# Kernel tuning notes

Measured on AMD Instinct MI355X. Metric: run time of the kernel, lower is better.

The kernel has to match this reference:

```python
import jax, jax.numpy as jnp
import numpy as np

B, N, D = 4, 1024, 1024
H, DH = 16, 64            # heads, dim_head; inner_dim = H*DH = D
CTX_N, CTX_D = 77, 768    # CLIP text context
FF_IN, FF_HID = 8 * D, 4 * D  # GEGLU: proj to 2*4*D, gate to 4*D
EPS = 1e-5
SCALE = DH ** -0.5
NL = 256                  # 2**8 levels for all quantizers
ZP_QKV = 128.0            # asymmetric 8-bit zero point for q/k/v
ZP_W = 0.0                # always_zero=True for softmax-weight quantizer


def _round_ste(t):
    return t + jax.lax.stop_gradient(jnp.round(t) - t)


def _fake_quant(x, delta, zp):
    xq = jnp.clip(_round_ste(x / delta) + zp, 0.0, NL - 1.0)
    return (xq - zp) * delta


def _ln(x, w, b):
    m = x.mean(-1, keepdims=True)
    v = x.var(-1, keepdims=True)
    return (x - m) * jax.lax.rsqrt(v + EPS) * w + b


def _split_heads(t):  # [b, n, h*d] -> [b, h, n, d]
    b, n, _ = t.shape
    return t.reshape(b, n, H, DH).transpose(0, 2, 1, 3)


def _attn(x, ctx, wq, wk, wv, wo, bo, dq, dk, dv, dw):
    q = _split_heads(x @ wq)
    k = _split_heads(ctx @ wk)
    v = _split_heads(ctx @ wv)
    qq = _fake_quant(q, dq, ZP_QKV)
    kk = _fake_quant(k, dk, ZP_QKV)
    sim = jnp.einsum('bhid,bhjd->bhij', qq, kk) * SCALE
    attn = jax.nn.softmax(sim, axis=-1)
    aw = _fake_quant(attn, dw, ZP_W)
    vv = _fake_quant(v, dv, ZP_QKV)
    out = jnp.einsum('bhij,bhjd->bhid', aw, vv)
    b, _, n, _ = out.shape
    out = out.transpose(0, 2, 1, 3).reshape(b, n, H * DH)
    return out @ wo + bo


def _geglu_ff(x, w1, b1, w2, b2):
    h = x @ w1 + b1
    a, g = jnp.split(h, 2, axis=-1)
    return (a * jax.nn.gelu(g, approximate=False)) @ w2 + b2


def setup_inputs() -> dict:
    key = jax.random.key(0)
    ks = jax.random.split(key, 16)
    w = lambda i, shp, s: jax.random.normal(ks[i], shp, jnp.float32) * s
    sD = D ** -0.5
    sC = CTX_D ** -0.5
    return {
        'x': jax.random.normal(ks[0], (B, N, D), jnp.float32),
        'context': jax.random.normal(ks[1], (B, CTX_N, CTX_D), jnp.float32),
        'norm1_w': jnp.ones((D,), jnp.float32), 'norm1_b': jnp.zeros((D,), jnp.float32),
        'norm2_w': jnp.ones((D,), jnp.float32), 'norm2_b': jnp.zeros((D,), jnp.float32),
        'norm3_w': jnp.ones((D,), jnp.float32), 'norm3_b': jnp.zeros((D,), jnp.float32),
        'a1_wq': w(2, (D, D), sD), 'a1_wk': w(3, (D, D), sD), 'a1_wv': w(4, (D, D), sD),
        'a1_wo': w(5, (D, D), sD), 'a1_bo': jnp.zeros((D,), jnp.float32),
        'a2_wq': w(6, (D, D), sD), 'a2_wk': w(7, (CTX_D, D), sC), 'a2_wv': w(8, (CTX_D, D), sC),
        'a2_wo': w(9, (D, D), sD), 'a2_bo': jnp.zeros((D,), jnp.float32),
        'ff_w1': w(10, (D, FF_IN), sD), 'ff_b1': jnp.zeros((FF_IN,), jnp.float32),
        'ff_w2': w(11, (FF_HID, D), FF_HID ** -0.5), 'ff_b2': jnp.zeros((D,), jnp.float32),
        'd1_q': jnp.asarray(0.02, jnp.float32), 'd1_k': jnp.asarray(0.02, jnp.float32),
        'd1_v': jnp.asarray(0.02, jnp.float32), 'd1_w': jnp.asarray(1.0 / 255.0, jnp.float32),
        'd2_q': jnp.asarray(0.02, jnp.float32), 'd2_k': jnp.asarray(0.02, jnp.float32),
        'd2_v': jnp.asarray(0.02, jnp.float32), 'd2_w': jnp.asarray(1.0 / 255.0, jnp.float32),
    }


def reference(x, context, norm1_w, norm1_b, norm2_w, norm2_b, norm3_w, norm3_b,
              a1_wq, a1_wk, a1_wv, a1_wo, a1_bo,
              a2_wq, a2_wk, a2_wv, a2_wo, a2_bo,
              ff_w1, ff_b1, ff_w2, ff_b2,
              d1_q, d1_k, d1_v, d1_w, d2_q, d2_k, d2_v, d2_w):
    # attn1: quantized self-attention
    x = _attn(_ln(x, norm1_w, norm1_b), _ln(x, norm1_w, norm1_b),
              a1_wq, a1_wk, a1_wv, a1_wo, a1_bo, d1_q, d1_k, d1_v, d1_w) + x
    # attn2: quantized cross-attention with text context
    x = _attn(_ln(x, norm2_w, norm2_b), context,
              a2_wq, a2_wk, a2_wv, a2_wo, a2_bo, d2_q, d2_k, d2_v, d2_w) + x
    # GEGLU feed-forward
    x = _geglu_ff(_ln(x, norm3_w, norm3_b), ff_w1, ff_b1, ff_w2, ff_b2) + x
    return x
```

## Files before the change

kernel.cpp:

```cpp
#include <hip/hip_runtime.h>
#include <math.h>


typedef unsigned short u16;
typedef __attribute__((ext_vector_type(8))) short short8;
typedef __attribute__((ext_vector_type(4))) float f32x4;

__device__ inline float b2f(u16 v) { return __uint_as_float(((unsigned)v) << 16); }
__device__ inline u16 f2b(float f) {
  unsigned u = __float_as_uint(f);
  unsigned r = u + 0x7fffu + ((u >> 16) & 1u);
  return (u16)(r >> 16);
}

__device__ inline void glds16(const u16* g, u16* l) {
  __builtin_amdgcn_global_load_lds(
      (const __attribute__((address_space(1))) void*)g,
      (__attribute__((address_space(3))) void*)l, 16, 0, 0);
}

__global__ __launch_bounds__(256) void transpose_k(const float* __restrict__ in,
                                                   u16* __restrict__ out,
                                                   int R, int C) {
  __shared__ float t[32][33];
  int tx = threadIdx.x & 31, ty = threadIdx.x >> 5;
  int c0 = blockIdx.x * 32, r0 = blockIdx.y * 32;
#pragma unroll
  for (int i = 0; i < 32; i += 8)
    t[ty + i][tx] = in[(size_t)(r0 + ty + i) * C + c0 + tx];
  __syncthreads();
#pragma unroll
  for (int i = 0; i < 32; i += 8)
    out[(size_t)(c0 + ty + i) * R + r0 + tx] = f2b(t[tx][ty + i]);
}

struct TrBatch { const float* in[4]; u16* out[4]; int R[4]; };
__global__ __launch_bounds__(256) void transpose4_k(TrBatch a) {
  int z = blockIdx.z;
  const float* in = a.in[z];
  u16* out = a.out[z];
  int R = a.R[z];
  int r0 = blockIdx.y * 32;
  if (r0 >= R) return;
  __shared__ float t[32][33];
  int tx = threadIdx.x & 31, ty = threadIdx.x >> 5;
  int c0 = blockIdx.x * 32;
#pragma unroll
  for (int i = 0; i < 32; i += 8)
    t[ty + i][tx] = in[(size_t)(r0 + ty + i) * 1024 + c0 + tx];
  __syncthreads();
#pragma unroll
  for (int i = 0; i < 32; i += 8)
    out[(size_t)(c0 + ty + i) * R + r0 + tx] = f2b(t[tx][ty + i]);
}

__global__ __launch_bounds__(256) void tr16_k(const u16* __restrict__ in,
                                              u16* __restrict__ out, int NK,
                                              int NKP) {
  __shared__ u16 t[32][33];
  int tx = threadIdx.x & 31, ty = threadIdx.x >> 5;
  int n0 = blockIdx.x * 32, c0 = blockIdx.y * 32, b = blockIdx.z;
  const u16* ib = in + (size_t)b * NK * 1024;
  u16* ob = out + (size_t)b * 1024 * NKP;
#pragma unroll
  for (int i = 0; i < 32; i += 8) {
    int n = n0 + ty + i;
    n = n < NK ? n : NK - 1;
    t[ty + i][tx] = ib[(size_t)n * 1024 + c0 + tx];
  }
  __syncthreads();
#pragma unroll
  for (int i = 0; i < 32; i += 8)
    ob[(size_t)(c0 + ty + i) * NKP + n0 + tx] = t[tx][ty + i];
}

__global__ __launch_bounds__(256) void cast_k(const float* __restrict__ in,
                                              u16* __restrict__ out) {
  int i = (blockIdx.x * 256 + threadIdx.x) * 4;
  float4 v = *(const float4*)(in + i);
  out[i + 0] = f2b(v.x);
  out[i + 1] = f2b(v.y);
  out[i + 2] = f2b(v.z);
  out[i + 3] = f2b(v.w);
}

__global__ __launch_bounds__(256) void ln_k(const float* __restrict__ X,
                                            const float* __restrict__ W,
                                            const float* __restrict__ Bi,
                                            u16* __restrict__ Out) {
  const int row = blockIdx.x, tid = threadIdx.x;
  float4 x = *(const float4*)(X + (size_t)row * 1024 + tid * 4);
  float s = x.x + x.y + x.z + x.w;
  float s2 = x.x * x.x + x.y * x.y + x.z * x.z + x.w * x.w;
#pragma unroll
  for (int off = 32; off >= 1; off >>= 1) {
    s += __shfl_down(s, off);
    s2 += __shfl_down(s2, off);
  }
  __shared__ float red[8];
  int wave = tid >> 6, lane = tid & 63;
  if (lane == 0) { red[wave] = s; red[4 + wave] = s2; }
  __syncthreads();
  s = red[0] + red[1] + red[2] + red[3];
  s2 = red[4] + red[5] + red[6] + red[7];
  float mean = s * 0.0009765625f;
  float var = s2 * 0.0009765625f - mean * mean;
  float rs = rsqrtf(var + 1e-5f);
  float4 w = *(const float4*)(W + tid * 4);
  float4 b = *(const float4*)(Bi + tid * 4);
  u16* orow = Out + (size_t)row * 1024 + tid * 4;
  orow[0] = f2b((x.x - mean) * rs * w.x + b.x);
  orow[1] = f2b((x.y - mean) * rs * w.y + b.y);
  orow[2] = f2b((x.z - mean) * rs * w.z + b.z);
  orow[3] = f2b((x.w - mean) * rs * w.w + b.w);
}

template <int EPI, int TM>
__global__ __launch_bounds__(256, 2) void gemm_bt(
    const u16* __restrict__ A, int lda, const u16* __restrict__ Bt, int ldb,
    void* __restrict__ Cp, int ldc, const float* __restrict__ bias,
    const float* __restrict__ res, int ldr, const float* __restrict__ dp,
    const float* __restrict__ dp2, const float* __restrict__ dp3,
    size_t segsz, int M, int N, int K) {
  __shared__ __align__(16) u16 As[TM * 64];
  __shared__ __align__(16) u16 Bs[128 * 64];
  const int tid = threadIdx.x;
  const int lane = tid & 63, wave = tid >> 6;
  const int qd = lane >> 4, cl = lane & 15;
  const int wm = (wave & 1) * (TM / 2), wn = (wave >> 1) << 6;
  const int m0 = blockIdx.x * TM, n0 = blockIdx.y * 128;

  f32x4 acc[TM / 32][4];
  const f32x4 zero = {0.f, 0.f, 0.f, 0.f};
#pragma unroll
  for (int i = 0; i < TM / 32; i++)
#pragma unroll
    for (int j = 0; j < 4; j++) acc[i][j] = zero;

  for (int k0 = 0; k0 < K; k0 += 64) {
    __syncthreads();
#pragma unroll
    for (int it = 0; it < TM / 32; ++it) {
      int ch = it * 256 + tid;
      int r = ch >> 3, cc = (ch & 7) << 3;
      int gr = m0 + r;
      gr = gr < M ? gr : M - 1;
      glds16(A + (size_t)gr * lda + k0 + cc, As + ch * 8);
    }
#pragma unroll
    for (int it = 0; it < 4; ++it) {
      int ch = it * 256 + tid;
      int r = ch >> 3, cc = (ch & 7) << 3;
      glds16(Bt + (size_t)(n0 + r) * ldb + k0 + cc, Bs + ch * 8);
    }
    __syncthreads();
#pragma unroll
    for (int ks = 0; ks < 64; ks += 32) {
      short8 af[TM / 32], bf[4];
#pragma unroll
      for (int t = 0; t < TM / 32; t++)
        af[t] = *(const short8*)(As + (wm + t * 16 + cl) * 64 + ks + qd * 8);
#pragma unroll
      for (int t = 0; t < 4; t++)
        bf[t] = *(const short8*)(Bs + (wn + t * 16 + cl) * 64 + ks + qd * 8);
#pragma unroll
      for (int mt = 0; mt < TM / 32; mt++)
#pragma unroll
        for (int nt = 0; nt < 4; nt++)
          acc[mt][nt] = __builtin_amdgcn_mfma_f32_16x16x32_bf16(
              af[mt], bf[nt], acc[mt][nt], 0, 0, 0);
    }
  }

  float dscale = 1.f;
  u16* qbase = (u16*)Cp;
  if constexpr (EPI == 0) dscale = 1.0f / dp[0];
  if constexpr (EPI == 2) {
    int seg = n0 >> 10;
    const float* ds = (seg == 0) ? dp : ((seg == 1) ? dp2 : dp3);
    dscale = 1.0f / ds[0];
    qbase = (u16*)Cp + (size_t)seg * segsz;
  }
#pragma unroll
  for (int mt = 0; mt < TM / 32; ++mt) {
#pragma unroll
    for (int r = 0; r < 4; ++r) {
      int row = m0 + wm + mt * 16 + qd * 4 + r;
      if (row >= M) continue;
#pragma unroll
      for (int nt = 0; nt < 4; ++nt) {
        int col = n0 + wn + nt * 16 + cl;
        float v = acc[mt][nt][r];
        if constexpr (EPI == 0) {
          float xq = rintf(v * dscale) + 128.f;
          xq = fminf(fmaxf(xq, 0.f), 255.f);
          qbase[(size_t)row * ldc + col] = f2b(xq - 128.f);
        } else if constexpr (EPI == 2) {
          float xq = rintf(v * dscale) + 128.f;
          xq = fminf(fmaxf(xq, 0.f), 255.f);
          qbase[(size_t)row * ldc + (col & 1023)] = f2b(xq - 128.f);
        } else {
          v += bias[col] + res[(size_t)row * ldr + col];
          ((float*)Cp)[(size_t)row * ldc + col] = v;
        }
      }
    }
  }
}

__global__ __launch_bounds__(256, 2) void ff1_geglu_k(
    const u16* __restrict__ A, const u16* __restrict__ W1t,
    const float* __restrict__ b1, u16* __restrict__ gg, int M) {
  __shared__ __align__(16) u16 As[128 * 64];
  __shared__ __align__(16) u16 Ba[64 * 64];
  __shared__ __align__(16) u16 Bg[64 * 64];
  const int tid = threadIdx.x;
  const int lane = tid & 63, wave = tid >> 6;
  const int qd = lane >> 4, cl = lane & 15;
  const int wm = (wave & 1) << 6, wn = (wave >> 1) << 5;
  const int m0 = blockIdx.x * 128, n0 = blockIdx.y * 64;

  f32x4 aca[4][2], acg[4][2];
  const f32x4 zero = {0.f, 0.f, 0.f, 0.f};
#pragma unroll
  for (int i = 0; i < 4; i++)
#pragma unroll
    for (int j = 0; j < 2; j++) { aca[i][j] = zero; acg[i][j] = zero; }

  for (int k0 = 0; k0 < 1024; k0 += 64) {
    __syncthreads();
#pragma unroll
    for (int it = 0; it < 4; ++it) {
      int ch = it * 256 + tid;
      int r = ch >> 3, cc = (ch & 7) << 3;
      glds16(A + (size_t)(m0 + r) * 1024 + k0 + cc, As + ch * 8);
    }
#pragma unroll
    for (int it = 0; it < 2; ++it) {
      int ch = it * 256 + tid;
      int r = ch >> 3, cc = (ch & 7) << 3;
      glds16(W1t + (size_t)(n0 + r) * 1024 + k0 + cc, Ba + ch * 8);
      glds16(W1t + (size_t)(4096 + n0 + r) * 1024 + k0 + cc, Bg + ch * 8);
    }
    __syncthreads();
#pragma unroll
    for (int ks = 0; ks < 64; ks += 32) {
      short8 af[4], ba[2], bg[2];
#pragma unroll
      for (int t = 0; t < 4; t++)
        af[t] = *(const short8*)(As + (wm + t * 16 + cl) * 64 + ks + qd * 8);
#pragma unroll
      for (int t = 0; t < 2; t++) {
        ba[t] = *(const short8*)(Ba + (wn + t * 16 + cl) * 64 + ks + qd * 8);
        bg[t] = *(const short8*)(Bg + (wn + t * 16 + cl) * 64 + ks + qd * 8);
      }
#pragma unroll
      for (int mt = 0; mt < 4; mt++)
#pragma unroll
        for (int nt = 0; nt < 2; nt++) {
          aca[mt][nt] = __builtin_amdgcn_mfma_f32_16x16x32_bf16(
              af[mt], ba[nt], aca[mt][nt], 0, 0, 0);
          acg[mt][nt] = __builtin_amdgcn_mfma_f32_16x16x32_bf16(
              af[mt], bg[nt], acg[mt][nt], 0, 0, 0);
        }
    }
  }
#pragma unroll
  for (int mt = 0; mt < 4; ++mt)
#pragma unroll
    for (int r = 0; r < 4; ++r) {
      int row = m0 + wm + mt * 16 + qd * 4 + r;
#pragma unroll
      for (int nt = 0; nt < 2; ++nt) {
        int col = n0 + wn + nt * 16 + cl;
        float a = aca[mt][nt][r] + b1[col];
        float g = acg[mt][nt][r] + b1[4096 + col];
        float ge = 0.5f * g * (1.0f + erff(g * 0.70710678118654752f));
        gg[(size_t)row * 4096 + col] = f2b(a * ge);
      }
    }
}

__global__ __launch_bounds__(256, 4) void attn_k(
    const u16* __restrict__ Q, const u16* __restrict__ Kb,
    const u16* __restrict__ VbT, u16* __restrict__ O,
    const float* dqp, const float* dkp, const float* dvp, const float* dwp,
    int NK, int NKP) {
  __shared__ __align__(16) u16 Ks[64 * 64];
  __shared__ __align__(16) u16 VTs[64 * 64];
  __shared__ __align__(16) u16 Ps[4][16 * 72];
  const int tid = threadIdx.x;
  const int lane = tid & 63, wave = tid >> 6;
  const int qd = lane >> 4, cl = lane & 15;
  const int b = blockIdx.z, h = blockIdx.y, qt = blockIdx.x;
  const float sscale = dqp[0] * dkp[0] * 0.125f;
  const float oscale = dwp[0] * dvp[0];
  const float inv_dw = 1.0f / dwp[0];
  const f32x4 zero = {0.f, 0.f, 0.f, 0.f};

  short8 qf[2][2];
#pragma unroll
  for (int g = 0; g < 2; ++g) {
    const u16* qrow =
        Q + (size_t)(b * 1024 + qt * 128 + g * 64 + wave * 16 + cl) * 1024 +
        h * 64;
    qf[g][0] = *(const short8*)(qrow + qd * 8);
    qf[g][1] = *(const short8*)(qrow + 32 + qd * 8);
  }

  const u16* kbase = Kb + (size_t)(b * NK) * 1024 + h * 64;
  const u16* vtbase = VbT + ((size_t)b * 1024 + h * 64) * NKP;
  const int r_st = tid >> 3, c_st = (tid & 7) << 3;

  float m_s[2] = {-1e30f, -1e30f}, l_s[2] = {0.f, 0.f};
  for (int j0 = 0; j0 < NK; j0 += 64) {
    __syncthreads();
#pragma unroll
    for (int it = 0; it < 2; ++it) {
      int r = it * 32 + r_st;
      int j = j0 + r;
      j = j < NK ? j : NK - 1;
      glds16(kbase + (size_t)j * 1024 + c_st, Ks + (it * 256 + tid) * 8);
    }
    __syncthreads();
    const bool full = (j0 + 64 <= NK);
#pragma unroll
    for (int g = 0; g < 2; ++g) {
      float sc[16];
#pragma unroll
      for (int nt = 0; nt < 4; ++nt) {
        short8 kf0 = *(const short8*)(Ks + (nt * 16 + cl) * 64 + qd * 8);
        short8 kf1 = *(const short8*)(Ks + (nt * 16 + cl) * 64 + 32 + qd * 8);
        f32x4 st = zero;
        st = __builtin_amdgcn_mfma_f32_16x16x32_bf16(kf0, qf[g][0], st, 0, 0, 0);
        st = __builtin_amdgcn_mfma_f32_16x16x32_bf16(kf1, qf[g][1], st, 0, 0, 0);
#pragma unroll
        for (int r = 0; r < 4; ++r) {
          int key = j0 + nt * 16 + qd * 4 + r;
          sc[nt * 4 + r] = (full || key < NK) ? st[r] * sscale : -1e30f;
        }
      }
      float mx = sc[0];
#pragma unroll
      for (int i = 1; i < 16; ++i) mx = fmaxf(mx, sc[i]);
      mx = fmaxf(mx, __shfl_xor(mx, 16));
      mx = fmaxf(mx, __shfl_xor(mx, 32));
      float mn = fmaxf(m_s[g], mx);
      float ss = 0.f;
#pragma unroll
      for (int i = 0; i < 16; ++i) ss += __expf(sc[i] - mn);
      ss += __shfl_xor(ss, 16);
      ss += __shfl_xor(ss, 32);
      l_s[g] = l_s[g] * __expf(m_s[g] - mn) + ss;
      m_s[g] = mn;
    }
  }
  float il_s[2] = {1.0f / l_s[0], 1.0f / l_s[1]};

  f32x4 oacc[2][4];
#pragma unroll
  for (int g = 0; g < 2; ++g)
#pragma unroll
    for (int t = 0; t < 4; t++) oacc[g][t] = zero;

  for (int j0 = 0; j0 < NK; j0 += 64) {
    __syncthreads();
#pragma unroll
    for (int it = 0; it < 2; ++it) {
      int r = it * 32 + r_st;
      int j = j0 + r;
      j = j < NK ? j : NK - 1;
      glds16(kbase + (size_t)j * 1024 + c_st, Ks + (it * 256 + tid) * 8);
      glds16(vtbase + (size_t)r * NKP + j0 + c_st, VTs + (it * 256 + tid) * 8);
    }
    __syncthreads();
    const bool full = (j0 + 64 <= NK);
#pragma unroll
    for (int g = 0; g < 2; ++g) {
#pragma unroll
      for (int nt = 0; nt < 4; ++nt) {
        short8 kf0 = *(const short8*)(Ks + (nt * 16 + cl) * 64 + qd * 8);
        short8 kf1 = *(const short8*)(Ks + (nt * 16 + cl) * 64 + 32 + qd * 8);
        f32x4 st = zero;
        st = __builtin_amdgcn_mfma_f32_16x16x32_bf16(kf0, qf[g][0], st, 0, 0, 0);
        st = __builtin_amdgcn_mfma_f32_16x16x32_bf16(kf1, qf[g][1], st, 0, 0, 0);
        u16 pk[4];
#pragma unroll
        for (int r = 0; r < 4; ++r) {
          int key = j0 + nt * 16 + qd * 4 + r;
          float aw = 0.f;
          if (full || key < NK) {
            float attn = __expf(st[r] * sscale - m_s[g]) * il_s[g];
            aw = fminf(fmaxf(rintf(attn * inv_dw), 0.f), 255.f);
          }
          pk[r] = f2b(aw);
        }
        uint2 pv;
        pv.x = (unsigned)pk[0] | ((unsigned)pk[1] << 16);
        pv.y = (unsigned)pk[2] | ((unsigned)pk[3] << 16);
        *(uint2*)(&Ps[wave][cl * 72 + nt * 16 + qd * 4]) = pv;
      }
#pragma unroll
      for (int ks = 0; ks < 2; ++ks) {
        short8 pf = *(const short8*)(&Ps[wave][cl * 72 + ks * 32 + qd * 8]);
#pragma unroll
        for (int dt = 0; dt < 4; ++dt) {
          short8 vf =
              *(const short8*)(VTs + (dt * 16 + cl) * 64 + ks * 32 + qd * 8);
          oacc[g][dt] = __builtin_amdgcn_mfma_f32_16x16x32_bf16(
              pf, vf, oacc[g][dt], 0, 0, 0);
        }
      }
    }
  }
#pragma unroll
  for (int g = 0; g < 2; ++g)
#pragma unroll
    for (int dt = 0; dt < 4; ++dt)
#pragma unroll
      for (int r = 0; r < 4; r++) {
        size_t addr = (size_t)(b * 1024 + qt * 128 + g * 64 + wave * 16 +
                               qd * 4 + r) * 1024 +
                      h * 64 + dt * 16 + cl;
        O[addr] = f2b(oacc[g][dt][r] * oscale);
      }
}

extern "C" void kernel_launch(void* const* d_in, const int* in_sizes, int n_in,
                              void* d_out, int out_size, void* d_ws,
                              size_t ws_size, hipStream_t stream) {
  (void)in_sizes; (void)n_in; (void)out_size; (void)ws_size;
  const float* x    = (const float*)d_in[0];
  const float* ctx  = (const float*)d_in[1];
  const float* n1w  = (const float*)d_in[2];
  const float* n1b  = (const float*)d_in[3];
  const float* n2w  = (const float*)d_in[4];
  const float* n2b  = (const float*)d_in[5];
  const float* n3w  = (const float*)d_in[6];
  const float* n3b  = (const float*)d_in[7];
  const float* a1wq = (const float*)d_in[8];
  const float* a1wk = (const float*)d_in[9];
  const float* a1wv = (const float*)d_in[10];
  const float* a1wo = (const float*)d_in[11];
  const float* a1bo = (const float*)d_in[12];
  const float* a2wq = (const float*)d_in[13];
  const float* a2wk = (const float*)d_in[14];
  const float* a2wv = (const float*)d_in[15];
  const float* a2wo = (const float*)d_in[16];
  const float* a2bo = (const float*)d_in[17];
  const float* ffw1 = (const float*)d_in[18];
  const float* ffb1 = (const float*)d_in[19];
  const float* ffw2 = (const float*)d_in[20];
  const float* ffb2 = (const float*)d_in[21];
  const float* d1q = (const float*)d_in[22];
  const float* d1k = (const float*)d_in[23];
  const float* d1v = (const float*)d_in[24];
  const float* d1w = (const float*)d_in[25];
  const float* d2q = (const float*)d_in[26];
  const float* d2k = (const float*)d_in[27];
  const float* d2v = (const float*)d_in[28];
  const float* d2w = (const float*)d_in[29];

  char* ws = (char*)d_ws;
  const size_t MB = 1u << 20;
  u16* W    = (u16*)(ws + 0 * MB);
  u16* lnb  = (u16*)(ws + 16 * MB);
  u16* qb   = (u16*)(ws + 24 * MB);
  u16* kb   = (u16*)(ws + 32 * MB);
  u16* vb   = (u16*)(ws + 40 * MB);
  u16* vbT  = (u16*)(ws + 48 * MB);
  u16* ao   = (u16*)(ws + 56 * MB);
  float* x1 = (float*)(ws + 64 * MB);
  u16* k2b  = (u16*)(ws + 32 * MB);
  u16* v2b  = k2b + 308 * 1024;
  u16* vbTc = (u16*)(ws + 34 * MB);
  u16* ctxb = (u16*)(ws + 35 * MB);
  u16* gg   = (u16*)(ws + 24 * MB);

  u16* WT0 = W;
  u16* WT1 = (u16*)(ws + 2 * MB);
  u16* WT2 = (u16*)(ws + 4 * MB);
  u16* WT3 = (u16*)(ws + 6 * MB);
  u16* WT3c = WT2 + 1024 * 768;

  dim3 T256(256);
  {
    TrBatch tb;
    tb.in[0] = a1wq; tb.out[0] = WT0; tb.R[0] = 1024;
    tb.in[1] = a1wk; tb.out[1] = WT1; tb.R[1] = 1024;
    tb.in[2] = a1wv; tb.out[2] = WT2; tb.R[2] = 1024;
    tb.in[3] = a1wo; tb.out[3] = WT3; tb.R[3] = 1024;
    transpose4_k<<<dim3(32, 32, 4), T256, 0, stream>>>(tb);
  }
  ln_k<<<4096, T256, 0, stream>>>(x, n1w, n1b, lnb);
  gemm_bt<2, 128><<<dim3(32, 24), T256, 0, stream>>>(
      lnb, 1024, WT0, 1024, qb, 1024, nullptr, nullptr, 0, d1q, d1k, d1v,
      (size_t)4096 * 1024, 4096, 3072, 1024);
  tr16_k<<<dim3(32, 32, 4), T256, 0, stream>>>(vb, vbT, 1024, 1024);
  attn_k<<<dim3(8, 16, 4), T256, 0, stream>>>(qb, kb, vbT, ao, d1q, d1k, d1v,
                                              d1w, 1024, 1024);
  gemm_bt<1, 64><<<dim3(64, 8), T256, 0, stream>>>(
      ao, 1024, WT3, 1024, x1, 1024, a1bo, x, 1024, nullptr, nullptr, nullptr,
      0, 4096, 1024, 1024);
  {
    TrBatch tb;
    tb.in[0] = a2wq; tb.out[0] = WT0; tb.R[0] = 1024;
    tb.in[1] = a2wo; tb.out[1] = WT1; tb.R[1] = 1024;
    tb.in[2] = a2wk; tb.out[2] = WT2;  tb.R[2] = 768;
    tb.in[3] = a2wv; tb.out[3] = WT3c; tb.R[3] = 768;
    transpose4_k<<<dim3(32, 32, 4), T256, 0, stream>>>(tb);
  }
  ln_k<<<4096, T256, 0, stream>>>(x1, n2w, n2b, lnb);
  cast_k<<<231, T256, 0, stream>>>(ctx, ctxb);
  gemm_bt<0, 64><<<dim3(64, 8), T256, 0, stream>>>(
      lnb, 1024, WT0, 1024, qb, 1024, nullptr, nullptr, 0, d2q, nullptr,
      nullptr, 0, 4096, 1024, 1024);
  gemm_bt<2, 64><<<dim3(5, 16), T256, 0, stream>>>(
      ctxb, 768, WT2, 768, k2b, 1024, nullptr, nullptr, 0, d2k, d2v, nullptr,
      (size_t)308 * 1024, 308, 2048, 768);
  tr16_k<<<dim3(3, 32, 4), T256, 0, stream>>>(v2b, vbTc, 77, 128);
  attn_k<<<dim3(8, 16, 4), T256, 0, stream>>>(qb, k2b, vbTc, ao, d2q, d2k, d2v,
                                              d2w, 77, 128);
  gemm_bt<1, 64><<<dim3(64, 8), T256, 0, stream>>>(
      ao, 1024, WT1, 1024, x1, 1024, a2bo, x1, 1024, nullptr, nullptr, nullptr,
      0, 4096, 1024, 1024);
  transpose_k<<<dim3(256, 32), T256, 0, stream>>>(ffw1, W, 1024, 8192);
  ln_k<<<4096, T256, 0, stream>>>(x1, n3w, n3b, lnb);
  ff1_geglu_k<<<dim3(32, 64), T256, 0, stream>>>(lnb, W, ffb1, gg, 4096);
  transpose_k<<<dim3(32, 128), T256, 0, stream>>>(ffw2, W, 4096, 1024);
  gemm_bt<1, 64><<<dim3(64, 8), T256, 0, stream>>>(
      gg, 4096, W, 4096, d_out, 1024, ffb2, x1, 1024, nullptr, nullptr,
      nullptr, 0, 4096, 1024, 4096);
}
```

Before: 586.6 us.

## Rewrite GEGLU FF1 GEMM as 256x256 tile double-buffered 8-wave pipelined kernel

Replaces the 128x64 (plus gate) FF1 GEGLU kernel with a 512-thread kernel that computes a 256-row by 128-value/128-gate tile. It double-buffers A and B in 128 KB of LDS, interleaving global-to-LDS loads for the next K tile with MFMA quadrants. It uses XOR-swizzled LDS layouts to avoid bank conflicts and explicit waitcnt, barriers, sched barriers and setprio. The goal is more data reuse per loaded tile and overlap of memory with compute. The cost is one block per CU, heavy register use, and fragile hand-tuned synchronisation.

```diff
diff --git a/kernel.cpp b/kernel.cpp
--- a/kernel.cpp
+++ b/kernel.cpp
@@ -208,77 +208,168 @@
   }
 }
 
-__global__ __launch_bounds__(256, 2) void ff1_geglu_k(
-    const u16* __restrict__ A, const u16* __restrict__ W1t,
-    const float* __restrict__ b1, u16* __restrict__ gg, int M) {
-  __shared__ __align__(16) u16 As[128 * 64];
-  __shared__ __align__(16) u16 Ba[64 * 64];
-  __shared__ __align__(16) u16 Bg[64 * 64];
+#define VMW(n) asm volatile("s_waitcnt vmcnt(" #n ")" ::: "memory")
+#define LGKM0() asm volatile("s_waitcnt lgkmcnt(0)" ::: "memory")
+#define SBAR() __builtin_amdgcn_s_barrier()
+#define SCHED0() __builtin_amdgcn_sched_barrier(0)
+
+#define ST_A(P, MH, K0)                                                      \
+  do {                                                                       \
+    _Pragma("unroll") for (int it = 0; it < 2; ++it) {                       \
+      int r_ = (MH) * 128 + it * 64 + sr;                                    \
+      glds16(Ag + (size_t)(m0 + r_) * 1024 + (K0) + ((sc ^ (r_ & 7)) << 3),  \
+             As + (P) * 16384 + r_ * 64 + (sc << 3));                        \
+    }                                                                        \
+  } while (0)
+
+#define ST_B(P, BH, K0)                                                      \
+  do {                                                                       \
+    _Pragma("unroll") for (int it = 0; it < 2; ++it) {                       \
+      int r_ = it * 64 + sr;                                                 \
+      glds16(W1t + (size_t)((BH) * 4096 + n0 + r_) * 1024 + (K0) +           \
+                 ((sc ^ (r_ & 7)) << 3),                                     \
+             Bs + (P) * 16384 + ((BH) * 128 + r_) * 64 + (sc << 3));         \
+    }                                                                        \
+  } while (0)
+
+#define RD_A(P, MH)                                                          \
+  do {                                                                       \
+    _Pragma("unroll") for (int mf = 0; mf < 4; ++mf) {                       \
+      int row_ = (MH) * 128 + wr * 64 + mf * 16 + cl;                        \
+      _Pragma("unroll") for (int ks = 0; ks < 2; ++ks)                       \
+        af[mf * 2 + ks] = *(const short8*)(As + (P) * 16384 + row_ * 64 +    \
+                                           (((ks * 4 + qd) ^ (cl & 7)) << 3)); \
+    }                                                                        \
+  } while (0)
+
+#define RD_B(P, NH)                                                          \
+  do {                                                                       \
+    _Pragma("unroll") for (int nf = 0; nf < 2; ++nf) {                       \
+      int j_ = (NH) * 128 + wc * 32 + nf * 16 + cl;                          \
+      _Pragma("unroll") for (int ks = 0; ks < 2; ++ks)                       \
+        bf[nf * 2 + ks] = *(const short8*)(Bs + (P) * 16384 + j_ * 64 +      \
+                                           (((ks * 4 + qd) ^ (cl & 7)) << 3)); \
+    }                                                                        \
+  } while (0)
+
+#define MFMA_Q(MH, NH)                                                       \
+  do {                                                                       \
+    _Pragma("unroll") for (int mf = 0; mf < 4; ++mf)                         \
+      _Pragma("unroll") for (int nf = 0; nf < 2; ++nf)                       \
+        _Pragma("unroll") for (int ks = 0; ks < 2; ++ks)                     \
+          acc[(MH) * 4 + mf][(NH) * 2 + nf] =                                \
+              __builtin_amdgcn_mfma_f32_16x16x32_bf16(                       \
+                  af[mf * 2 + ks], bf[nf * 2 + ks],                          \
+                  acc[(MH) * 4 + mf][(NH) * 2 + nf], 0, 0, 0);               \
+  } while (0)
+
+#define KTILE(P, KN, LAST)                                                   \
+  do {                                                                       \
+                                            \
+    RD_A(P, 0);                                                              \
+    RD_B(P, 0);                                                              \
+    if (!(LAST)) ST_A((P) ^ 1, 0, KN);                                       \
+    SBAR();                                                                  \
+    LGKM0();                                                                 \
+    SCHED0();                                                                \
+    __builtin_amdgcn_s_setprio(1);                                           \
+    MFMA_Q(0, 0);                                                            \
+    __builtin_amdgcn_s_setprio(0);                                           \
+    SCHED0();                                                                \
+    if (!(LAST)) { VMW(4); } else { VMW(2); }                                \
+    SBAR();                                                                  \
+                              \
+    RD_A(P, 1);                                                              \
+    if (!(LAST)) ST_B((P) ^ 1, 0, KN);                                       \
+    SBAR();                                                                  \
+    LGKM0();                                                                 \
+    SCHED0();                                                                \
+    __builtin_amdgcn_s_setprio(1);                                           \
+    MFMA_Q(1, 0);                                                            \
+    __builtin_amdgcn_s_setprio(0);                                           \
+    SCHED0();                                                                \
+    if (!(LAST)) { VMW(4); } else { VMW(0); }                                \
+    SBAR();                                                                  \
+                              \
+    RD_B(P, 1);                                                              \
+    if (!(LAST)) ST_A((P) ^ 1, 1, KN);                                       \
+    SBAR();                                                                  \
+    LGKM0();                                                                 \
+    SCHED0();                                                                \
+    __builtin_amdgcn_s_setprio(1);                                           \
+    MFMA_Q(1, 1);                                                            \
+    __builtin_amdgcn_s_setprio(0);                                           \
+    SCHED0();                                                                \
+    SBAR();                                                                  \
+             \
+    RD_A(P, 0);                                                              \
+    if (!(LAST)) ST_B((P) ^ 1, 1, KN);                                       \
+    SBAR();                                                                  \
+    LGKM0();                                                                 \
+    SCHED0();                                                                \
+    __builtin_amdgcn_s_setprio(1);                                           \
+    MFMA_Q(0, 1);                                                            \
+    __builtin_amdgcn_s_setprio(0);                                           \
+    SCHED0();                                                                \
+    if (!(LAST)) { VMW(4); }                                                 \
+    SBAR();                                                                  \
+  } while (0)
+
+__global__ __launch_bounds__(512, 1) void ff1_geglu8_k(
+    const u16* __restrict__ Ag, const u16* __restrict__ W1t,
+    const float* __restrict__ b1, u16* __restrict__ gg) {
+  __shared__ __align__(16) u16 smem[65536];
+  u16* As = smem;
+  u16* Bs = smem + 32768;
   const int tid = threadIdx.x;
   const int lane = tid & 63, wave = tid >> 6;
   const int qd = lane >> 4, cl = lane & 15;
-  const int wm = (wave & 1) << 6, wn = (wave >> 1) << 5;
-  const int m0 = blockIdx.x * 128, n0 = blockIdx.y * 64;
-
-  f32x4 aca[4][2], acg[4][2];
+  const int wr = wave >> 2, wc = wave & 3;
+  const int m0 = blockIdx.x * 256;
+  const int n0 = blockIdx.y * 128;
+  const int sr = tid >> 3, sc = tid & 7;
+
+  f32x4 acc[8][4];
   const f32x4 zero = {0.f, 0.f, 0.f, 0.f};
 #pragma unroll
-  for (int i = 0; i < 4; i++)
-#pragma unroll
-    for (int j = 0; j < 2; j++) { aca[i][j] = zero; acg[i][j] = zero; }
-
-  for (int k0 = 0; k0 < 1024; k0 += 64) {
-    __syncthreads();
-#pragma unroll
-    for (int it = 0; it < 4; ++it) {
-      int ch = it * 256 + tid;
-      int r = ch >> 3, cc = (ch & 7) << 3;
-      glds16(A + (size_t)(m0 + r) * 1024 + k0 + cc, As + ch * 8);
-    }
-#pragma unroll
-    for (int it = 0; it < 2; ++it) {
-      int ch = it * 256 + tid;
-      int r = ch >> 3, cc = (ch & 7) << 3;
-      glds16(W1t + (size_t)(n0 + r) * 1024 + k0 + cc, Ba + ch * 8);
-      glds16(W1t + (size_t)(4096 + n0 + r) * 1024 + k0 + cc, Bg + ch * 8);
-    }
-    __syncthreads();
-#pragma unroll
-    for (int ks = 0; ks < 64; ks += 32) {
-      short8 af[4], ba[2], bg[2];
-#pragma unroll
-      for (int t = 0; t < 4; t++)
-        af[t] = *(const short8*)(As + (wm + t * 16 + cl) * 64 + ks + qd * 8);
-#pragma unroll
-      for (int t = 0; t < 2; t++) {
-        ba[t] = *(const short8*)(Ba + (wn + t * 16 + cl) * 64 + ks + qd * 8);
-        bg[t] = *(const short8*)(Bg + (wn + t * 16 + cl) * 64 + ks + qd * 8);
+  for (int i = 0; i < 8; ++i)
+#pragma unroll
+    for (int j = 0; j < 4; ++j) acc[i][j] = zero;
+  short8 af[8], bf[4];
+
+  ST_A(0, 0, 0);
+  ST_B(0, 0, 0);
+  ST_A(0, 1, 0);
+  ST_B(0, 1, 0);
+  VMW(4);
+  SBAR();
+  SCHED0();
+
+  int p = 0;
+#pragma unroll 1
+  for (int t = 0; t < 15; ++t) {
+    KTILE(p, (t + 1) * 64, 0);
+    p ^= 1;
+  }
+  KTILE(1, 0, 1);
+
+#pragma unroll
+  for (int i = 0; i < 8; ++i) {
+    const int row = m0 + (i >> 2) * 128 + wr * 64 + (i & 3) * 16 + qd * 4;
+#pragma unroll
+    for (int nf = 0; nf < 2; ++nf) {
+      const int col = n0 + wc * 32 + nf * 16 + cl;
+      const float ba = b1[col];
+      const float bg = b1[4096 + col];
+#pragma unroll
+      for (int r = 0; r < 4; ++r) {
+        float a = acc[i][nf][r] + ba;
+        float g = acc[i][2 + nf][r] + bg;
+        float ge = 0.5f * g * (1.0f + erff(g * 0.70710678118654752f));
+        gg[(size_t)(row + r) * 4096 + col] = f2b(a * ge);
       }
-#pragma unroll
-      for (int mt = 0; mt < 4; mt++)
-#pragma unroll
-        for (int nt = 0; nt < 2; nt++) {
-          aca[mt][nt] = __builtin_amdgcn_mfma_f32_16x16x32_bf16(
-              af[mt], ba[nt], aca[mt][nt], 0, 0, 0);
-          acg[mt][nt] = __builtin_amdgcn_mfma_f32_16x16x32_bf16(
-              af[mt], bg[nt], acg[mt][nt], 0, 0, 0);
-        }
-    }
-  }
-#pragma unroll
-  for (int mt = 0; mt < 4; ++mt)
-#pragma unroll
-    for (int r = 0; r < 4; ++r) {
-      int row = m0 + wm + mt * 16 + qd * 4 + r;
-#pragma unroll
-      for (int nt = 0; nt < 2; ++nt) {
-        int col = n0 + wn + nt * 16 + cl;
-        float a = aca[mt][nt][r] + b1[col];
-        float g = acg[mt][nt][r] + b1[4096 + col];
-        float ge = 0.5f * g * (1.0f + erff(g * 0.70710678118654752f));
-        gg[(size_t)row * 4096 + col] = f2b(a * ge);
-      }
-    }
+    }
+  }
 }
 
 __global__ __launch_bounds__(256, 4) void attn_k(
@@ -526,7 +617,7 @@
       0, 4096, 1024, 1024);
   transpose_k<<<dim3(256, 32), T256, 0, stream>>>(ffw1, W, 1024, 8192);
   ln_k<<<4096, T256, 0, stream>>>(x1, n3w, n3b, lnb);
-  ff1_geglu_k<<<dim3(32, 64), T256, 0, stream>>>(lnb, W, ffb1, gg, 4096);
+  ff1_geglu8_k<<<dim3(16, 32), dim3(512), 0, stream>>>(lnb, W, ffb1, gg);
   transpose_k<<<dim3(32, 128), T256, 0, stream>>>(ffw2, W, 4096, 1024);
   gemm_bt<1, 64><<<dim3(64, 8), T256, 0, stream>>>(
       gg, 4096, W, 4096, d_out, 1024, ffb2, x1, 1024, nullptr, nullptr,
```

New measurement: 578.5 us. Within noise of the previous version (-1.4%).
